# Kernel optimization log

Measured on AMD Instinct MI355X. Metric: run time of the kernel, lower is better.

The kernel has to match this reference:

```python
import jax, jax.numpy as jnp
import numpy as np
import math

B, T, C = 8, 4096, 768
N_LAYER, LAYER_ID = 12, 6
LN_EPS = 1e-5


def wkv(w, u, k, v):
    """Numerically-stable RWKV-4 WKV recurrence.
    w, u: [C] (per-channel decay / bonus); k, v: [B, T, C] -> y: [B, T, C]."""
    kT = jnp.swapaxes(k, 0, 1)  # [T, B, C]
    vT = jnp.swapaxes(v, 0, 1)

    def step(carry, kv):
        aa, bb, pp = carry
        kt, vt = kv
        ww = u + kt
        p = jnp.maximum(pp, ww)
        e1 = jnp.exp(pp - p)
        e2 = jnp.exp(ww - p)
        y = (e1 * aa + e2 * vt) / (e1 * bb + e2)
        ww2 = w + pp
        p2 = jnp.maximum(ww2, kt)
        e1b = jnp.exp(ww2 - p2)
        e2b = jnp.exp(kt - p2)
        return (e1b * aa + e2b * vt, e1b * bb + e2b, p2), y

    zeros = jnp.zeros((k.shape[0], k.shape[2]), k.dtype)
    init = (zeros, zeros, jnp.full_like(zeros, -1e38))
    _, yT = jax.lax.scan(step, init, (kT, vT))
    return jnp.swapaxes(yT, 0, 1)  # [B, T, C]


def setup_inputs():
    key = jax.random.key(0)
    ks = jax.random.split(key, 8)
    # fancy init of spatial_decay / spatial_first (matches torch __init__)
    ratio = LAYER_ID / max(N_LAYER - 1, 1)
    h = np.arange(C, dtype=np.float64)
    decay = -5 + 8 * (h / max(C - 1, 1)) ** (0.7 + 1.3 * ratio)
    zigzag = np.array([(i + 1) % 3 - 1 for i in range(C)], dtype=np.float64) * 0.5
    first = np.ones(C) * math.log(0.3) + zigzag
    s = C ** -0.5
    return {
        "x_seq": jax.random.normal(ks[0], (B, T, C), jnp.float32),
        "scan_indices": jax.random.permutation(ks[1], T).astype(jnp.int32),
        "spatial_decay": jnp.asarray(decay, jnp.float32),
        "spatial_first": jnp.asarray(first, jnp.float32),
        "Wk": jax.random.normal(ks[2], (C, C), jnp.float32) * s,
        "Wv": jax.random.normal(ks[3], (C, C), jnp.float32) * s,
        "Wr": jax.random.normal(ks[4], (C, C), jnp.float32) * s,
        "Wo": jax.random.normal(ks[5], (C, C), jnp.float32) * s,
        "ln_g": jnp.ones((C,), jnp.float32),
        "ln_b": jnp.zeros((C,), jnp.float32),
    }


def reference(x_seq, scan_indices, spatial_decay, spatial_first, Wk, Wv, Wr, Wo, ln_g, ln_b):
    L = x_seq.shape[1]
    k = jnp.einsum('blc,dc->bld', x_seq, Wk)
    v = jnp.einsum('blc,dc->bld', x_seq, Wv)
    r = jnp.einsum('blc,dc->bld', x_seq, Wr)
    sr = jax.nn.sigmoid(r)
    # gather along sequence per scan order
    k_s = jnp.take(k, scan_indices, axis=1)
    v_s = jnp.take(v, scan_indices, axis=1)
    rwkv = wkv(spatial_decay / L, spatial_first / L, k_s, v_s)
    inv = jnp.argsort(scan_indices)
    rwkv = jnp.take(rwkv, inv, axis=1)
    # LayerNorm (key_norm)
    mu = jnp.mean(rwkv, axis=-1, keepdims=True)
    var = jnp.var(rwkv, axis=-1, keepdims=True)
    rwkv = (rwkv - mu) * jax.lax.rsqrt(var + LN_EPS) * ln_g + ln_b
    rwkv = sr * rwkv
    return jnp.einsum('blc,dc->bld', rwkv, Wo)
```

## Files before the change

kernel.cpp:

```cpp
#include <hip/hip_runtime.h>
#include <cstddef>
#include <cstdint>

#define B_DIM 8
#define T_SEQ 4096
#define C_DIM 768
#define M_ROWS (B_DIM * T_SEQ)
#define CC (C_DIM * C_DIM)
#define NCH 32
#define CHL (T_SEQ / NCH)

using bf16x8 = __attribute__((ext_vector_type(8))) short;
using f32x4  = __attribute__((ext_vector_type(4))) float;

static __device__ __forceinline__ unsigned short f2bf(float f) {
  unsigned int u = __float_as_uint(f);
  return (unsigned short)((u + 0x7fffu + ((u >> 16) & 1u)) >> 16);
}
static __device__ __forceinline__ float bf2f(unsigned short s) {
  return __uint_as_float(((unsigned int)s) << 16);
}

static __device__ __forceinline__ void gload_lds16(const void* g, void* l) {
  __builtin_amdgcn_global_load_lds(
      (const __attribute__((address_space(1))) unsigned int*)g,
      (__attribute__((address_space(3))) unsigned int*)l, 16, 0, 0);
}

__global__ __launch_bounds__(256) void convert_x(
    const float4* __restrict__ x, ushort4* __restrict__ xh)
{
  int i = blockIdx.x * 256 + threadIdx.x;
  float4 v = x[i];
  ushort4 h;
  h.x = f2bf(v.x); h.y = f2bf(v.y); h.z = f2bf(v.z); h.w = f2bf(v.w);
  xh[i] = h;
}

__global__ __launch_bounds__(256) void convert_w4(
    const float4* __restrict__ w0, const float4* __restrict__ w1,
    const float4* __restrict__ w2, const float4* __restrict__ w3,
    ushort4* __restrict__ dst)
{
  const int z = blockIdx.y;
  const float4* __restrict__ src = (z == 0) ? w0 : (z == 1) ? w1 : (z == 2) ? w2 : w3;
  int i = blockIdx.x * 256 + threadIdx.x;
  float4 v = src[i];
  ushort4 h;
  h.x = f2bf(v.x); h.y = f2bf(v.y); h.z = f2bf(v.z); h.w = f2bf(v.w);
  dst[(size_t)z * (CC / 4) + i] = h;
}

#define STG_A(DBYTE, TAU, KH) do {                                        \
    const int ko_ = (TAU) * 64 + (KH) * 32;                               \
    short* d_ = lds + (((DBYTE) + (KH) * 16384) >> 1);                    \
    gload_lds16(pA0 + ko_, d_ + ub0 * 8);                                 \
    gload_lds16(pA1 + ko_, d_ + ub1 * 8);                                 \
  } while (0)
#define STG_B(DBYTE, TAU, KH) do {                                        \
    const int ko_ = (TAU) * 64 + (KH) * 32;                               \
    short* d_ = lds + (((DBYTE) + 32768 + (KH) * 16384) >> 1);            \
    gload_lds16(pW0 + ko_, d_ + ub0 * 8);                                 \
    gload_lds16(pW1 + ko_, d_ + ub1 * 8);                                 \
  } while (0)

#define PHASE(DB, KH, MQ, READB, STAGE, CKPT)                             \
  {                                                                        \
    _Pragma("unroll")                                                      \
    for (int mi = 0; mi < 4; ++mi)                                         \
      a[mi] = *(const bf16x8*)(lds +                                       \
          (((DB) + (KH) * 16384 + aoff + ((MQ) * 4 + mi) * 256) >> 1));    \
    if (READB) {                                                           \
      _Pragma("unroll")                                                    \
      for (int ni = 0; ni < 4; ++ni)                                       \
        b[ni] = *(const bf16x8*)(lds +                                     \
            (((DB) + (KH) * 16384 + boff + ni * 256) >> 1));               \
    }                                                                      \
    STAGE;                                                                 \
    __builtin_amdgcn_s_barrier();                                          \
    asm volatile("s_waitcnt lgkmcnt(0)" ::: "memory");                     \
    __builtin_amdgcn_sched_barrier(0);                                     \
    __builtin_amdgcn_s_setprio(1);                                         \
    _Pragma("unroll")                                                      \
    for (int mi = 0; mi < 4; ++mi)                                         \
      _Pragma("unroll")                                                    \
      for (int ni = 0; ni < 4; ++ni)                                       \
        acc[(MQ) * 4 + mi][ni] = __builtin_amdgcn_mfma_f32_16x16x32_bf16(  \
            a[mi], b[ni], acc[(MQ) * 4 + mi][ni], 0, 0, 0);                \
    __builtin_amdgcn_s_setprio(0);                                         \
    CKPT;                                                                  \
    __builtin_amdgcn_s_barrier();                                          \
  }

template<int MODE>
__global__ __launch_bounds__(512, 2) void gemm8p(
    const short* __restrict__ A, const short* __restrict__ Wb,
    unsigned short* __restrict__ OK, unsigned short* __restrict__ OV,
    unsigned short* __restrict__ OSR, float* __restrict__ Oout)
{
  extern __shared__ short lds[];
  const int K = C_DIM;
  constexpr int NWN = (MODE == 0) ? 9 : 3;
  constexpr int CPX = (MODE == 0) ? 144 : 48;

  int f  = blockIdx.x + blockIdx.y * NWN;
  int wg = (f & 7) * CPX + (f >> 3);
  const int n0 = (wg % NWN) * 256;
  const int m0 = (wg / NWN) * 256;

  const int tid  = threadIdx.x;
  const int lane = tid & 63, wave = tid >> 6;
  const int wr = wave >> 2, wc = wave & 3;
  const int lr = lane & 15, lk = lane >> 4;

  const int aoff = lk * 4096 + wr * 2048 + lr * 16;
  const int boff = 32768 + lk * 4096 + wc * 1024 + lr * 16;

  const int ub0 = wave * 128;
  const int ub1 = wave * 128 + 64;
  const int r0 = (ub0 & 255) + lane, q0 = ub0 >> 8;
  const int r1 = (ub1 & 255) + lane, q1 = ub1 >> 8;
  const short* pA0 = A  + (size_t)(m0 + r0) * K + q0 * 8;
  const short* pA1 = A  + (size_t)(m0 + r1) * K + q1 * 8;
  const short* pW0 = Wb + (size_t)(n0 + r0) * K + q0 * 8;
  const short* pW1 = Wb + (size_t)(n0 + r1) * K + q1 * 8;

  f32x4 acc[8][4];
#pragma unroll
  for (int i = 0; i < 8; ++i)
#pragma unroll
    for (int j = 0; j < 4; ++j) acc[i][j] = (f32x4){0.f, 0.f, 0.f, 0.f};

  STG_A(0, 0, 0); STG_B(0, 0, 0); STG_A(0, 0, 1); STG_B(0, 0, 1);
  STG_A(65536, 1, 0); STG_B(65536, 1, 0); STG_A(65536, 1, 1); STG_B(65536, 1, 1);
  asm volatile("s_waitcnt vmcnt(8)" ::: "memory");
  __builtin_amdgcn_s_barrier();

  bf16x8 a[4], b[4];
  for (int it = 0; it < 6; ++it) {
    PHASE(0, 0, 0, 1, if (it >= 1) STG_A(65536, 2 * it + 1, 1), )
    PHASE(0, 0, 1, 0, if (it >= 1) STG_B(65536, 2 * it + 1, 1), )
    PHASE(0, 1, 0, 1, if (it < 5) STG_A(0, 2 * it + 2, 0), )
    PHASE(0, 1, 1, 0, if (it < 5) STG_B(0, 2 * it + 2, 0),
          if (it < 5) { asm volatile("s_waitcnt vmcnt(4)" ::: "memory"); }
          else       { asm volatile("s_waitcnt vmcnt(0)" ::: "memory"); })
    PHASE(65536, 0, 0, 1, if (it < 5) STG_A(0, 2 * it + 2, 1), )
    PHASE(65536, 0, 1, 0, if (it < 5) STG_B(0, 2 * it + 2, 1), )
    PHASE(65536, 1, 0, 1, if (it < 5) STG_A(65536, 2 * it + 3, 0), )
    PHASE(65536, 1, 1, 0, if (it < 5) STG_B(65536, 2 * it + 3, 0),
          if (it < 5) { asm volatile("s_waitcnt vmcnt(4)" ::: "memory"); })
  }

  if (MODE == 0) {
    const int which = n0 / 768;
    const int nc = (n0 % 768) + wc * 64;
    unsigned short* __restrict__ D = (which == 0) ? OK : (which == 1) ? OV : OSR;
#pragma unroll
    for (int mi = 0; mi < 8; ++mi)
#pragma unroll
      for (int ni = 0; ni < 4; ++ni) {
        const int row = m0 + wr * 128 + mi * 16 + lk * 4;
        const int col = nc + ni * 16 + lr;
#pragma unroll
        for (int j = 0; j < 4; ++j) {
          float v = acc[mi][ni][j];
          if (which == 2) v = 1.f / (1.f + __expf(-v));
          D[(size_t)(row + j) * C_DIM + col] = f2bf(v);
        }
      }
  } else {
#pragma unroll
    for (int mi = 0; mi < 8; ++mi)
#pragma unroll
      for (int ni = 0; ni < 4; ++ni) {
        const int row = m0 + wr * 128 + mi * 16 + lk * 4;
        const int col = n0 + wc * 64 + ni * 16 + lr;
#pragma unroll
        for (int j = 0; j < 4; ++j)
          Oout[(size_t)(row + j) * C_DIM + col] = acc[mi][ni][j];
      }
  }
}

#define P1_LOAD(kk_, vv_, base_)                                  \
  _Pragma("unroll") for (int j = 0; j < 8; ++j) {                 \
    int r_ = si[(base_) + j];                                     \
    kk_[j] = Kb[(size_t)r_ * C_DIM];                              \
    vv_[j] = Vb[(size_t)r_ * C_DIM];                              \
  }
#define P1_COMP(kk_, vv_)                                         \
  _Pragma("unroll") for (int j = 0; j < 8; ++j) {                 \
    float kt = bf2f(kk_[j]), vt = bf2f(vv_[j]);                   \
    float ww2 = w + pp; float p2 = fmaxf(ww2, kt);                \
    float e1b = __expf(ww2 - p2), e2b = __expf(kt - p2);          \
    aa = e1b * aa + e2b * vt; bb = e1b * bb + e2b; pp = p2;       \
  }

__global__ __launch_bounds__(256) void wkv_pass1(
    const unsigned short* __restrict__ Kin, const unsigned short* __restrict__ Vin,
    const int* __restrict__ sidx, const float* __restrict__ decay,
    float* __restrict__ aL, float* __restrict__ bL, float* __restrict__ pL)
{
  __shared__ int si[CHL];
  const int tid = threadIdx.x;
  const int ch = blockIdx.x, b = blockIdx.z;
  const int c = blockIdx.y * 256 + tid;
  if (tid < CHL) si[tid] = sidx[ch * CHL + tid];
  __syncthreads();
  const float w = decay[c] * (1.0f / (float)T_SEQ);
  const unsigned short* Kb = Kin + (size_t)b * T_SEQ * C_DIM + c;
  const unsigned short* Vb = Vin + (size_t)b * T_SEQ * C_DIM + c;
  float aa = 0.f, bb = 0.f, pp = -1e38f;
  unsigned short kA[8], vA[8], kB[8], vB[8];
  P1_LOAD(kA, vA, 0)
  for (int t0 = 0; t0 < CHL; t0 += 16) {
    P1_LOAD(kB, vB, t0 + 8)
    P1_COMP(kA, vA)
    if (t0 + 16 < CHL) { P1_LOAD(kA, vA, t0 + 16) }
    P1_COMP(kB, vB)
  }
  const int idx = (b * C_DIM + c) * NCH + ch;
  aL[idx] = aa; bL[idx] = bb; pL[idx] = pp;
}

__global__ __launch_bounds__(256) void wkv_scan(
    const float* __restrict__ aL, const float* __restrict__ bL,
    const float* __restrict__ pL,
    float* __restrict__ aI, float* __restrict__ bI, float* __restrict__ pI,
    const float* __restrict__ decay)
{
  const int g = blockIdx.x * 256 + threadIdx.x;
  const int c = g % C_DIM;
  const float wL = decay[c] * ((float)CHL / (float)T_SEQ);
  float aa = 0.f, bb = 0.f, pp = -1e38f;
  const int base = g * NCH;
  for (int ch = 0; ch < NCH; ++ch) {
    aI[base + ch] = aa; bI[base + ch] = bb; pI[base + ch] = pp;
    float p1 = pp + wL;
    float p2 = pL[base + ch];
    float p  = fmaxf(p1, p2);
    float e1 = __expf(p1 - p), e2 = __expf(p2 - p);
    aa = e1 * aa + e2 * aL[base + ch];
    bb = e1 * bb + e2 * bL[base + ch];
    pp = p;
  }
}

#define P2_LOAD(rr_, kk_, vv_, base_)                             \
  _Pragma("unroll") for (int j = 0; j < 8; ++j) {                 \
    int r_ = si[(base_) + j];                                     \
    rr_[j] = r_;                                                  \
    kk_[j] = Kb[(size_t)r_ * C_DIM];                              \
    vv_[j] = Vb[(size_t)r_ * C_DIM];                              \
  }
#define P2_COMP(rr_, kk_, vv_)                                    \
  _Pragma("unroll") for (int j = 0; j < 8; ++j) {                 \
    float kt = bf2f(kk_[j]), vt = bf2f(vv_[j]);                   \
    float ww = u + kt; float p = fmaxf(pp, ww);                   \
    float e1 = __expf(pp - p), e2 = __expf(ww - p);               \
    float y = (e1 * aa + e2 * vt) / (e1 * bb + e2);               \
    Yb[(size_t)rr_[j] * C_DIM] = f2bf(y);                         \
    float ww2 = w + pp; float p2 = fmaxf(ww2, kt);                \
    float e1b = __expf(ww2 - p2), e2b = __expf(kt - p2);          \
    aa = e1b * aa + e2b * vt; bb = e1b * bb + e2b; pp = p2;       \
  }

__global__ __launch_bounds__(256) void wkv_pass2(
    const unsigned short* __restrict__ Kin, const unsigned short* __restrict__ Vin,
    const int* __restrict__ sidx,
    const float* __restrict__ decay, const float* __restrict__ first,
    const float* __restrict__ aI, const float* __restrict__ bI,
    const float* __restrict__ pI, unsigned short* __restrict__ Y)
{
  __shared__ int si[CHL];
  const int tid = threadIdx.x;
  const int ch = blockIdx.x, b = blockIdx.z;
  const int c = blockIdx.y * 256 + tid;
  if (tid < CHL) si[tid] = sidx[ch * CHL + tid];
  __syncthreads();
  const float w = decay[c] * (1.0f / (float)T_SEQ);
  const float u = first[c] * (1.0f / (float)T_SEQ);
  const unsigned short* Kb = Kin + (size_t)b * T_SEQ * C_DIM + c;
  const unsigned short* Vb = Vin + (size_t)b * T_SEQ * C_DIM + c;
  unsigned short* Yb = Y + (size_t)b * T_SEQ * C_DIM + c;
  const int idx = (b * C_DIM + c) * NCH + ch;
  float aa = aI[idx], bb = bI[idx], pp = pI[idx];
  int rA[8], rB[8]; unsigned short kA[8], vA[8], kB[8], vB[8];
  P2_LOAD(rA, kA, vA, 0)
  for (int t0 = 0; t0 < CHL; t0 += 16) {
    P2_LOAD(rB, kB, vB, t0 + 8)
    P2_COMP(rA, kA, vA)
    if (t0 + 16 < CHL) { P2_LOAD(rA, kA, vA, t0 + 16) }
    P2_COMP(rB, kB, vB)
  }
}

__global__ __launch_bounds__(256) void ln_gate(
    const unsigned short* __restrict__ Y, const unsigned short* __restrict__ SR,
    const float* __restrict__ gam, const float* __restrict__ bet,
    unsigned short* __restrict__ G)
{
  const size_t row = blockIdx.x;
  const unsigned short* x = Y + row * C_DIM;
  const unsigned short* sr = SR + row * C_DIM;
  unsigned short* go = G + row * C_DIM;
  const int tid = threadIdx.x;

  float vals[3];
  float s = 0.f, s2 = 0.f;
#pragma unroll
  for (int j = 0; j < 3; ++j) {
    float v = bf2f(x[tid + j * 256]);
    vals[j] = v;
    s += v; s2 += v * v;
  }
#pragma unroll
  for (int off = 32; off >= 1; off >>= 1) {
    s  += __shfl_xor(s, off, 64);
    s2 += __shfl_xor(s2, off, 64);
  }
  __shared__ float red[8];
  const int wid = tid >> 6;
  if ((tid & 63) == 0) { red[wid] = s; red[wid + 4] = s2; }
  __syncthreads();
  s  = red[0] + red[1] + red[2] + red[3];
  s2 = red[4] + red[5] + red[6] + red[7];

  const float mu   = s * (1.f / (float)C_DIM);
  const float var  = s2 * (1.f / (float)C_DIM) - mu * mu;
  const float rsig = rsqrtf(var + 1e-5f);

#pragma unroll
  for (int j = 0; j < 3; ++j) {
    const int cc = tid + j * 256;
    float yv = (vals[j] - mu) * rsig * gam[cc] + bet[cc];
    go[cc] = f2bf(yv * bf2f(sr[cc]));
  }
}

extern "C" void kernel_launch(void* const* d_in, const int* in_sizes, int n_in,
                              void* d_out, int out_size, void* d_ws, size_t ws_size,
                              hipStream_t stream) {
  const float* x     = (const float*)d_in[0];
  const int*   sidx  = (const int*)  d_in[1];
  const float* decay = (const float*)d_in[2];
  const float* first = (const float*)d_in[3];
  const float* Wk    = (const float*)d_in[4];
  const float* Wv    = (const float*)d_in[5];
  const float* Wr    = (const float*)d_in[6];
  const float* Wo    = (const float*)d_in[7];
  const float* ln_g  = (const float*)d_in[8];
  const float* ln_b  = (const float*)d_in[9];
  float* out = (float*)d_out;

  const size_t NE = (size_t)M_ROWS * C_DIM;
  short* Whs  = (short*)d_ws;
  short* x_hi = Whs + 4 * (size_t)CC;
  unsigned short* Ybuf = (unsigned short*)x_hi;
  unsigned short* Kbuf = (unsigned short*)(x_hi + NE);
  unsigned short* Gbuf = Kbuf;
  unsigned short* Vbuf = Kbuf + NE;
  unsigned short* SRb  = Vbuf + NE;
  float* aL = (float*)(SRb + NE);
  float* bL = aL + 196608;
  float* pL = bL + 196608;
  float* aI = pL + 196608;
  float* bI = aI + 196608;
  float* pI = bI + 196608;

  (void)hipFuncSetAttribute(reinterpret_cast<const void*>(&gemm8p<0>),
                            hipFuncAttributeMaxDynamicSharedMemorySize, 131072);
  (void)hipFuncSetAttribute(reinterpret_cast<const void*>(&gemm8p<1>),
                            hipFuncAttributeMaxDynamicSharedMemorySize, 131072);

  convert_x<<<24576, 256, 0, stream>>>((const float4*)x, (ushort4*)x_hi);
  convert_w4<<<dim3(576, 4), 256, 0, stream>>>(
      (const float4*)Wk, (const float4*)Wv, (const float4*)Wr, (const float4*)Wo,
      (ushort4*)Whs);

  gemm8p<0><<<dim3(9, 128), 512, 131072, stream>>>(
      x_hi, Whs, Kbuf, Vbuf, SRb, nullptr);

  wkv_pass1<<<dim3(NCH, 3, B_DIM), 256, 0, stream>>>(Kbuf, Vbuf, sidx, decay, aL, bL, pL);
  wkv_scan<<<24, 256, 0, stream>>>(aL, bL, pL, aI, bI, pI, decay);
  wkv_pass2<<<dim3(NCH, 3, B_DIM), 256, 0, stream>>>(Kbuf, Vbuf, sidx, decay, first,
                                                     aI, bI, pI, Ybuf);
  ln_gate<<<M_ROWS, 256, 0, stream>>>(Ybuf, SRb, ln_g, ln_b, Gbuf);
  gemm8p<1><<<dim3(3, 128), 512, 131072, stream>>>(
      (const short*)Gbuf, Whs + 3 * (size_t)CC, nullptr, nullptr, nullptr, out);
}
```

Before: 386.7 us.

## Load GEMM B operand directly into registers and triple-buffer A in LDS

The GEMM kernel now stages only the A tile through LDS, using a three-slot ring buffer with prefetch two tiles ahead. Each wave loads its B-operand fragments straight from global memory into double-buffered registers, one tile ahead. This removes LDS traffic and barriers for B and drops dynamic LDS from 128 KB to 96 KB. In exchange it uses more registers, and B loads are no longer shared across waves through LDS, so the same weight rows are fetched from global/L2 by several waves.

```diff
diff --git a/kernel.cpp b/kernel.cpp
--- a/kernel.cpp
+++ b/kernel.cpp
@@ -51,49 +51,63 @@
   dst[(size_t)z * (CC / 4) + i] = h;
 }
 
-#define STG_A(DBYTE, TAU, KH) do {                                        \
-    const int ko_ = (TAU) * 64 + (KH) * 32;                               \
-    short* d_ = lds + (((DBYTE) + (KH) * 16384) >> 1);                    \
-    gload_lds16(pA0 + ko_, d_ + ub0 * 8);                                 \
-    gload_lds16(pA1 + ko_, d_ + ub1 * 8);                                 \
-  } while (0)
-#define STG_B(DBYTE, TAU, KH) do {                                        \
-    const int ko_ = (TAU) * 64 + (KH) * 32;                               \
-    short* d_ = lds + (((DBYTE) + 32768 + (KH) * 16384) >> 1);            \
-    gload_lds16(pW0 + ko_, d_ + ub0 * 8);                                 \
-    gload_lds16(pW1 + ko_, d_ + ub1 * 8);                                 \
-  } while (0)
-
-#define PHASE(DB, KH, MQ, READB, STAGE, CKPT)                             \
+#define LOADB(DST, T) do { if ((T) < 12) {                                 \
+    _Pragma("unroll")                                                      \
+    for (int kh_ = 0; kh_ < 2; ++kh_) {                                    \
+      _Pragma("unroll")                                                    \
+      for (int ni_ = 0; ni_ < 4; ++ni_)                                    \
+        DST[kh_][ni_] = *(const bf16x8*)(pB[ni_] + (T) * 64 + kh_ * 32);   \
+    }                                                                      \
+  } } while (0)
+
+#define STAGEA(T) do { if ((T) < 12) {                                     \
+    short* d0_ = lds + ((T) % 3) * 16384 + wave * 2048;                    \
+    const int ko_ = (T) * 64;                                              \
+    gload_lds16(pA0 + ko_, d0_);                                           \
+    gload_lds16(pA1 + ko_, d0_ + 512);                                     \
+    gload_lds16(pA2 + ko_, d0_ + 1024);                                    \
+    gload_lds16(pA3 + ko_, d0_ + 1536);                                    \
+  } } while (0)
+
+#define SUBPH(T, KH, MQ, CUR)                                              \
   {                                                                        \
-    _Pragma("unroll")                                                      \
-    for (int mi = 0; mi < 4; ++mi)                                         \
-      a[mi] = *(const bf16x8*)(lds +                                       \
-          (((DB) + (KH) * 16384 + aoff + ((MQ) * 4 + mi) * 256) >> 1));    \
-    if (READB) {                                                           \
-      _Pragma("unroll")                                                    \
-      for (int ni = 0; ni < 4; ++ni)                                       \
-        b[ni] = *(const bf16x8*)(lds +                                     \
-            (((DB) + (KH) * 16384 + boff + ni * 256) >> 1));               \
-    }                                                                      \
-    STAGE;                                                                 \
-    __builtin_amdgcn_s_barrier();                                          \
+    const short* ab_ = lds + ((T) % 3) * 16384 + (KH) * 8192 + ard + (MQ) * 512; \
+    bf16x8 a0_ = *(const bf16x8*)(ab_);                                    \
+    bf16x8 a1_ = *(const bf16x8*)(ab_ + 128);                              \
+    bf16x8 a2_ = *(const bf16x8*)(ab_ + 256);                              \
+    bf16x8 a3_ = *(const bf16x8*)(ab_ + 384);                              \
     asm volatile("s_waitcnt lgkmcnt(0)" ::: "memory");                     \
     __builtin_amdgcn_sched_barrier(0);                                     \
     __builtin_amdgcn_s_setprio(1);                                         \
     _Pragma("unroll")                                                      \
-    for (int mi = 0; mi < 4; ++mi)                                         \
-      _Pragma("unroll")                                                    \
-      for (int ni = 0; ni < 4; ++ni)                                       \
-        acc[(MQ) * 4 + mi][ni] = __builtin_amdgcn_mfma_f32_16x16x32_bf16(  \
-            a[mi], b[ni], acc[(MQ) * 4 + mi][ni], 0, 0, 0);                \
+    for (int ni_ = 0; ni_ < 4; ++ni_) {                                    \
+      acc[(MQ)*4+0][ni_] = __builtin_amdgcn_mfma_f32_16x16x32_bf16(        \
+          a0_, CUR[KH][ni_], acc[(MQ)*4+0][ni_], 0, 0, 0);                 \
+      acc[(MQ)*4+1][ni_] = __builtin_amdgcn_mfma_f32_16x16x32_bf16(        \
+          a1_, CUR[KH][ni_], acc[(MQ)*4+1][ni_], 0, 0, 0);                 \
+      acc[(MQ)*4+2][ni_] = __builtin_amdgcn_mfma_f32_16x16x32_bf16(        \
+          a2_, CUR[KH][ni_], acc[(MQ)*4+2][ni_], 0, 0, 0);                 \
+      acc[(MQ)*4+3][ni_] = __builtin_amdgcn_mfma_f32_16x16x32_bf16(        \
+          a3_, CUR[KH][ni_], acc[(MQ)*4+3][ni_], 0, 0, 0);                 \
+    }                                                                      \
     __builtin_amdgcn_s_setprio(0);                                         \
-    CKPT;                                                                  \
+  }
+
+#define TILE(T, CUR, NXT, LAST)                                            \
+  {                                                                        \
+    if (LAST) { asm volatile("s_waitcnt vmcnt(0)" ::: "memory"); }         \
+    else      { asm volatile("s_waitcnt vmcnt(4)" ::: "memory"); }         \
     __builtin_amdgcn_s_barrier();                                          \
+    __builtin_amdgcn_sched_barrier(0);                                     \
+    LOADB(NXT, (T) + 1);                                                   \
+    STAGEA((T) + 2);                                                       \
+    __builtin_amdgcn_sched_barrier(0);                                     \
+    SUBPH(T, 0, 0, CUR) SUBPH(T, 0, 1, CUR)                                \
+    SUBPH(T, 1, 0, CUR) SUBPH(T, 1, 1, CUR)                                \
   }
 
 template<int MODE>
-__global__ __launch_bounds__(512, 2) void gemm8p(
+__global__ __launch_bounds__(512, 2) void gemmRB(
     const short* __restrict__ A, const short* __restrict__ Wb,
     unsigned short* __restrict__ OK, unsigned short* __restrict__ OV,
     unsigned short* __restrict__ OSR, float* __restrict__ Oout)
@@ -113,17 +127,22 @@
   const int wr = wave >> 2, wc = wave & 3;
   const int lr = lane & 15, lk = lane >> 4;
 
-  const int aoff = lk * 4096 + wr * 2048 + lr * 16;
-  const int boff = 32768 + lk * 4096 + wc * 1024 + lr * 16;
-
-  const int ub0 = wave * 128;
-  const int ub1 = wave * 128 + 64;
-  const int r0 = (ub0 & 255) + lane, q0 = ub0 >> 8;
-  const int r1 = (ub1 & 255) + lane, q1 = ub1 >> 8;
-  const short* pA0 = A  + (size_t)(m0 + r0) * K + q0 * 8;
-  const short* pA1 = A  + (size_t)(m0 + r1) * K + q1 * 8;
-  const short* pW0 = Wb + (size_t)(n0 + r0) * K + q0 * 8;
-  const short* pW1 = Wb + (size_t)(n0 + r1) * K + q1 * 8;
+  const int ard = lk * 2048 + (wr * 128 + lr) * 8;
+
+  const int w4l = wave * 4;
+  const short* pA0 = A + (size_t)(m0 + ((w4l + 0) & 3) * 64 + lane) * K
+                     + ((w4l + 0) >> 4) * 32 + (((w4l + 0) >> 2) & 3) * 8;
+  const short* pA1 = A + (size_t)(m0 + ((w4l + 1) & 3) * 64 + lane) * K
+                     + ((w4l + 1) >> 4) * 32 + (((w4l + 1) >> 2) & 3) * 8;
+  const short* pA2 = A + (size_t)(m0 + ((w4l + 2) & 3) * 64 + lane) * K
+                     + ((w4l + 2) >> 4) * 32 + (((w4l + 2) >> 2) & 3) * 8;
+  const short* pA3 = A + (size_t)(m0 + ((w4l + 3) & 3) * 64 + lane) * K
+                     + ((w4l + 3) >> 4) * 32 + (((w4l + 3) >> 2) & 3) * 8;
+
+  const short* pB[4];
+#pragma unroll
+  for (int ni = 0; ni < 4; ++ni)
+    pB[ni] = Wb + (size_t)(n0 + wc * 64 + ni * 16 + lr) * K + lk * 8;
 
   f32x4 acc[8][4];
 #pragma unroll
@@ -131,24 +150,16 @@
 #pragma unroll
     for (int j = 0; j < 4; ++j) acc[i][j] = (f32x4){0.f, 0.f, 0.f, 0.f};
 
-  STG_A(0, 0, 0); STG_B(0, 0, 0); STG_A(0, 0, 1); STG_B(0, 0, 1);
-  STG_A(65536, 1, 0); STG_B(65536, 1, 0); STG_A(65536, 1, 1); STG_B(65536, 1, 1);
-  asm volatile("s_waitcnt vmcnt(8)" ::: "memory");
-  __builtin_amdgcn_s_barrier();
-
-  bf16x8 a[4], b[4];
+  bf16x8 bA[2][4], bB2[2][4];
+
+  STAGEA(0);
+  LOADB(bA, 0);
+  STAGEA(1);
+
   for (int it = 0; it < 6; ++it) {
-    PHASE(0, 0, 0, 1, if (it >= 1) STG_A(65536, 2 * it + 1, 1), )
-    PHASE(0, 0, 1, 0, if (it >= 1) STG_B(65536, 2 * it + 1, 1), )
-    PHASE(0, 1, 0, 1, if (it < 5) STG_A(0, 2 * it + 2, 0), )
-    PHASE(0, 1, 1, 0, if (it < 5) STG_B(0, 2 * it + 2, 0),
-          if (it < 5) { asm volatile("s_waitcnt vmcnt(4)" ::: "memory"); }
-          else       { asm volatile("s_waitcnt vmcnt(0)" ::: "memory"); })
-    PHASE(65536, 0, 0, 1, if (it < 5) STG_A(0, 2 * it + 2, 1), )
-    PHASE(65536, 0, 1, 0, if (it < 5) STG_B(0, 2 * it + 2, 1), )
-    PHASE(65536, 1, 0, 1, if (it < 5) STG_A(65536, 2 * it + 3, 0), )
-    PHASE(65536, 1, 1, 0, if (it < 5) STG_B(65536, 2 * it + 3, 0),
-          if (it < 5) { asm volatile("s_waitcnt vmcnt(4)" ::: "memory"); })
+    const int t0 = 2 * it;
+    TILE(t0, bA, bB2, 0)
+    TILE(t0 + 1, bB2, bA, (it == 5))
   }
 
   if (MODE == 0) {
@@ -368,17 +379,17 @@
   float* bI = aI + 196608;
   float* pI = bI + 196608;
 
-  (void)hipFuncSetAttribute(reinterpret_cast<const void*>(&gemm8p<0>),
-                            hipFuncAttributeMaxDynamicSharedMemorySize, 131072);
-  (void)hipFuncSetAttribute(reinterpret_cast<const void*>(&gemm8p<1>),
-                            hipFuncAttributeMaxDynamicSharedMemorySize, 131072);
+  (void)hipFuncSetAttribute(reinterpret_cast<const void*>(&gemmRB<0>),
+                            hipFuncAttributeMaxDynamicSharedMemorySize, 98304);
+  (void)hipFuncSetAttribute(reinterpret_cast<const void*>(&gemmRB<1>),
+                            hipFuncAttributeMaxDynamicSharedMemorySize, 98304);
 
   convert_x<<<24576, 256, 0, stream>>>((const float4*)x, (ushort4*)x_hi);
   convert_w4<<<dim3(576, 4), 256, 0, stream>>>(
       (const float4*)Wk, (const float4*)Wv, (const float4*)Wr, (const float4*)Wo,
       (ushort4*)Whs);
 
-  gemm8p<0><<<dim3(9, 128), 512, 131072, stream>>>(
+  gemmRB<0><<<dim3(9, 128), 512, 98304, stream>>>(
       x_hi, Whs, Kbuf, Vbuf, SRb, nullptr);
 
   wkv_pass1<<<dim3(NCH, 3, B_DIM), 256, 0, stream>>>(Kbuf, Vbuf, sidx, decay, aL, bL, pL);
@@ -386,6 +397,6 @@
   wkv_pass2<<<dim3(NCH, 3, B_DIM), 256, 0, stream>>>(Kbuf, Vbuf, sidx, decay, first,
                                                      aI, bI, pI, Ybuf);
   ln_gate<<<M_ROWS, 256, 0, stream>>>(Ybuf, SRb, ln_g, ln_b, Gbuf);
-  gemm8p<1><<<dim3(3, 128), 512, 131072, stream>>>(
+  gemmRB<1><<<dim3(3, 128), 512, 98304, stream>>>(
       (const short*)Gbuf, Whs + 3 * (size_t)CC, nullptr, nullptr, nullptr, out);
 }
```

Measured after the change: 444.3 us. +14.9%, slower.
